# Kernel optimization log

Measured on AMD Instinct MI355X. Metric: run time of the kernel, lower is better.

Reference implementation:

```python
import jax, jax.numpy as jnp
import numpy as np

N = 50000
E = 800000
DESC = 256
IN_CH = DESC + 64  # 320
HEADS = 4
HC = 64  # hidden_channels // heads
HID = HEADS * HC  # 256


def _lin(k, fan_in, fan_out):
    kw, kb = jax.random.split(k)
    s = 1.0 / np.sqrt(fan_in)
    W = jax.random.uniform(kw, (fan_in, fan_out), minval=-s, maxval=s, dtype=jnp.float32)
    b = jax.random.uniform(kb, (fan_out,), minval=-s, maxval=s, dtype=jnp.float32)
    return W, b


def setup_inputs() -> dict:
    key = jax.random.key(0)
    ks = jax.random.split(key, 16)
    x = jax.random.normal(ks[0], (N, DESC), dtype=jnp.float32)
    kpts = jax.random.uniform(ks[1], (N, 2), dtype=jnp.float32) * jnp.array([1216.0, 352.0])
    pts_3d = jax.random.uniform(ks[2], (N, 3), dtype=jnp.float32) * 10.0
    edge_index = jax.random.randint(ks[3], (2, E), 0, N, dtype=jnp.int64)

    W1, b1 = _lin(ks[4], 3, 32)
    W2, b2 = _lin(ks[5], 32, 64)
    Wres, bres = _lin(ks[6], IN_CH, HID)
    Wl, bl = _lin(ks[7], IN_CH, HID)
    Wr, br = _lin(ks[8], IN_CH, HID)
    We, _ = _lin(ks[9], 3, HID)
    att = jax.random.normal(ks[10], (HEADS, HC), dtype=jnp.float32) * 0.1
    conv_bias = jnp.zeros((HID,), dtype=jnp.float32)
    gamma = jnp.ones((HID,), dtype=jnp.float32)
    beta = jnp.zeros((HID,), dtype=jnp.float32)
    Wp, bp = _lin(ks[11], HID, 256)
    return dict(x=x, kpts=kpts, pts_3d=pts_3d, edge_index=edge_index,
                W1=W1, b1=b1, W2=W2, b2=b2, Wres=Wres, bres=bres,
                Wl=Wl, bl=bl, Wr=Wr, br=br, We=We, att=att, conv_bias=conv_bias,
                gamma=gamma, beta=beta, Wp=Wp, bp=bp)


def reference(x, kpts, pts_3d, edge_index, W1, b1, W2, b2, Wres, bres,
              Wl, bl, Wr, br, We, att, conv_bias, gamma, beta, Wp, bp):
    n = x.shape[0]
    norm_uv = kpts / jnp.array([1216.0, 352.0], dtype=kpts.dtype)
    depth = pts_3d[:, 2:3]
    pos_input = jnp.concatenate([norm_uv, depth], axis=-1)  # [N,3]
    pos_feat = jax.nn.silu(pos_input @ W1 + b1) @ W2 + b2   # [N,64]
    node_x = jnp.concatenate([x, pos_feat], axis=-1)        # [N,320]

    src, dst = edge_index[0], edge_index[1]
    rel_uv = norm_uv[dst] - norm_uv[src]                    # [E,2]
    dist = jnp.linalg.norm(rel_uv, axis=-1, keepdims=True)  # [E,1]
    edge_attr = jnp.concatenate([rel_uv, dist], axis=-1)    # [E,3]

    identity = node_x @ Wres + bres                         # [N,256]

    # GATv2Conv (share_weights=False, concat=True, neg_slope=0.2, no self-loops)
    x_l = (node_x @ Wl + bl).reshape(n, HEADS, HC)
    x_r = (node_x @ Wr + br).reshape(n, HEADS, HC)
    e_feat = (edge_attr @ We).reshape(-1, HEADS, HC)        # [E,H,C]

    m = x_l[src] + x_r[dst] + e_feat                        # [E,H,C]
    m = jnp.where(m >= 0, m, 0.2 * m)                       # LeakyReLU(0.2)
    logits = jnp.einsum('ehc,hc->eh', m, att)               # [E,H]

    # segment softmax over incoming edges of each dst node
    lmax = jax.ops.segment_max(logits, dst, num_segments=n)  # [N,H]
    ex = jnp.exp(logits - lmax[dst])
    denom = jax.ops.segment_sum(ex, dst, num_segments=n)     # [N,H]
    alpha = ex / (denom[dst] + 1e-16)                        # [E,H]

    msg = x_l[src] * alpha[:, :, None]                       # [E,H,C]
    out = jax.ops.segment_sum(msg, dst, num_segments=n).reshape(n, HID) + conv_bias

    # LayerNorm
    mu = out.mean(-1, keepdims=True)
    var = out.var(-1, keepdims=True)
    out = (out - mu) / jnp.sqrt(var + 1e-5) * gamma + beta

    out = jax.nn.silu(out)
    out = out + identity
    out = out @ Wp + bp
    return out, alpha
```

## Files before the change

### kernel.cpp

```cpp
#include <hip/hip_runtime.h>
#include <math.h>

#define NN 50000
#define NPAD 50048
#define EE 800000
#define HIDC 256
#define INCH 320

typedef __attribute__((ext_vector_type(8))) short bf16x8;
typedef __attribute__((ext_vector_type(4))) float f32x4;
typedef __attribute__((ext_vector_type(2))) float f32x2;

static __device__ __forceinline__ float4 ld4(const float* p){ return *(const float4*)p; }

static __device__ __forceinline__ unsigned short f2b(float f){
  union { float f; unsigned u; } v; v.f = f;
  unsigned r = v.u + 0x7fffu + ((v.u >> 16) & 1u);
  return (unsigned short)(r >> 16);
}
static __device__ __forceinline__ float b2f(unsigned short u){
  union { unsigned u; float f; } v; v.u = ((unsigned)u) << 16; return v.f;
}
static __device__ __forceinline__ float rlane_f(float v, int l){
  return __uint_as_float(__builtin_amdgcn_readlane(__float_as_uint(v), l));
}
static __device__ __forceinline__ int rlane_i(int v, int l){
  return __builtin_amdgcn_readlane(v, l);
}
static __device__ __forceinline__ f32x2 unpk(unsigned u){
  f32x2 r;
  r.x = __uint_as_float(u << 16);
  r.y = __uint_as_float(u & 0xffff0000u);
  return r;
}
static __device__ __forceinline__ f32x2 fma2(f32x2 a, f32x2 b, f32x2 c){
  return __builtin_elementwise_fma(a, b, c);
}
static __device__ __forceinline__ f32x2 max2(f32x2 a, f32x2 b){
  return __builtin_elementwise_max(a, b);
}
static __device__ __forceinline__ f32x2 set2(float v){ f32x2 r; r.x = v; r.y = v; return r; }

typedef const __attribute__((address_space(1))) unsigned int* gas_u32;
typedef __attribute__((address_space(3))) unsigned int* las_u32;
static __device__ __forceinline__ void gload_lds16(const void* g, void* l){
  __builtin_amdgcn_global_load_lds((gas_u32)g, (las_u32)l, 16, 0, 0);
}

__global__ void cvt_x_kernel(const float* __restrict__ x, unsigned short* __restrict__ nodex)
{
  int t = blockIdx.x*blockDim.x + threadIdx.x;
  int row = t >> 6;
  if (row >= NN) return;
  int c4 = (t & 63) * 4;
  float4 v = ld4(x + (size_t)row*256 + c4);
  ushort4 o;
  o.x = f2b(v.x); o.y = f2b(v.y); o.z = f2b(v.z); o.w = f2b(v.w);
  *(ushort4*)(nodex + (size_t)row*320 + c4) = o;
}

__global__ void node_mlp_kernel(const float* __restrict__ kpts,
                                const float* __restrict__ pts3d,
                                const float* __restrict__ W1, const float* __restrict__ b1,
                                const float* __restrict__ W2, const float* __restrict__ b2,
                                unsigned short* __restrict__ nodex,
                                float* __restrict__ nuv)
{
  int i = blockIdx.x*blockDim.x + threadIdx.x;
  if (i >= NN) return;
  float u = kpts[2*i]   * (1.0f/1216.0f);
  float v = kpts[2*i+1] * (1.0f/352.0f);
  float d = pts3d[3*i+2];
  float2 uv; uv.x = u; uv.y = v;
  *(float2*)(nuv + 2*i) = uv;
  float h[32];
#pragma unroll
  for (int j=0;j<32;++j){
    float t = u*W1[j] + v*W1[32+j] + d*W1[64+j] + b1[j];
    h[j] = t / (1.0f + __expf(-t));
  }
  for (int o=0;o<64;o+=4){
    float s0=b2[o], s1=b2[o+1], s2=b2[o+2], s3=b2[o+3];
#pragma unroll
    for (int j=0;j<32;++j){
      float hj = h[j];
      const float* w = W2 + j*64 + o;
      s0 += hj*w[0]; s1 += hj*w[1]; s2 += hj*w[2]; s3 += hj*w[3];
    }
    ushort4 r; r.x=f2b(s0); r.y=f2b(s1); r.z=f2b(s2); r.w=f2b(s3);
    *(ushort4*)(nodex + (size_t)i*320 + 256 + o) = r;
  }
}

__global__ void cvt_w_kernel(const float* __restrict__ Wres, const float* __restrict__ Wl,
                             const float* __restrict__ Wr,   const float* __restrict__ Wp,
                             const float* __restrict__ bres, const float* __restrict__ bl,
                             const float* __restrict__ br,
                             unsigned short* __restrict__ wt, float* __restrict__ biascat)
{
  int t = blockIdx.x*blockDim.x + threadIdx.x;
  if (t < 245760) {
    int which = t / 81920;
    int rem = t % 81920;
    int n = rem / 320, k = rem % 320;
    const float* W = (which == 0) ? Wres : (which == 1) ? Wl : Wr;
    wt[(size_t)which*81920 + rem] = f2b(W[(size_t)k*256 + n]);
  } else if (t < 311296) {
    int r = t - 245760;
    int n = r / 256, k = r % 256;
    wt[245760 + r] = f2b(Wp[(size_t)k*256 + n]);
  } else {
    int r = t - 311296;
    const float* src = (r < 256) ? bres : (r < 512) ? bl : br;
    biascat[r] = src[r & 255];
  }
}

#define GK 64
__global__ __launch_bounds__(256) void mfma_gemm_kernel(
    const unsigned short* __restrict__ A,
    const unsigned short* __restrict__ BT,
    const float* __restrict__ bias,
    float* __restrict__ Cf,
    unsigned short* __restrict__ Cx1,
    unsigned short* __restrict__ Cx2,
    int M, int K)
{
  __shared__ unsigned short Als[128*GK];
  __shared__ unsigned short Bls[128*GK];
  int tid = threadIdx.x;
  int lane = tid & 63, wave = tid >> 6;
  int wm = (wave >> 1) * 64, wn = (wave & 1) * 64;
  int row0 = blockIdx.y * 128, col0 = blockIdx.x * 128;

  f32x4 acc[4][4];
#pragma unroll
  for (int i=0;i<4;++i)
#pragma unroll
    for (int j=0;j<4;++j){ acc[i][j].x=0.f; acc[i][j].y=0.f; acc[i][j].z=0.f; acc[i][j].w=0.f; }

  int fm = lane & 15;
  int q4 = lane >> 4;

  for (int k0 = 0; k0 < K; k0 += GK) {
#pragma unroll
    for (int it = 0; it < 4; ++it) {
      int cgl = it*256 + tid;
      int r = cgl >> 3;
      int kb = ((cgl ^ r) & 7) * 8;
      gload_lds16(A  + (size_t)(row0 + r)*K + k0 + kb, Als + (it*256 + wave*64)*8);
      gload_lds16(BT + (size_t)(col0 + r)*K + k0 + kb, Bls + (it*256 + wave*64)*8);
    }
    __syncthreads();

#pragma unroll
    for (int kk = 0; kk < 2; ++kk) {
      int j = kk*4 + q4;
      bf16x8 af[4], bfr[4];
#pragma unroll
      for (int mi=0; mi<4; ++mi){
        int row = wm + mi*16 + fm;
        af[mi] = *(const bf16x8*)&Als[row*GK + ((j ^ row) & 7)*8];
      }
#pragma unroll
      for (int ni=0; ni<4; ++ni){
        int row = wn + ni*16 + fm;
        bfr[ni] = *(const bf16x8*)&Bls[row*GK + ((j ^ row) & 7)*8];
      }
#pragma unroll
      for (int mi=0; mi<4; ++mi)
#pragma unroll
        for (int ni=0; ni<4; ++ni)
          acc[mi][ni] = __builtin_amdgcn_mfma_f32_16x16x32_bf16(af[mi], bfr[ni], acc[mi][ni], 0, 0, 0);
    }
    __syncthreads();
  }

  int seg = col0 >> 8;
  int colbase = col0 - seg*256;
  int cn = lane & 15, cr = (lane >> 4) * 4;
#pragma unroll
  for (int ni=0; ni<4; ++ni){
    int gcol = col0 + wn + ni*16 + cn;
    int col  = colbase + wn + ni*16 + cn;
    float bb = bias[gcol];
#pragma unroll
    for (int mi=0; mi<4; ++mi){
#pragma unroll
      for (int r=0; r<4; ++r){
        int row = row0 + wm + mi*16 + cr + r;
        if (row < M){
          float v = acc[mi][ni][r] + bb;
          if (seg == 0)      Cf [(size_t)row*256 + col] = v;
          else if (seg == 1) Cx1[(size_t)row*256 + col] = f2b(v);
          else               Cx2[(size_t)row*256 + col] = f2b(v);
        }
      }
    }
  }
}

__global__ void hist_kernel(const int* __restrict__ ei, int* __restrict__ deg){
  int e = blockIdx.x*blockDim.x + threadIdx.x;
  if (e < EE) atomicAdd(&deg[ei[EE + e]], 1);
}

__global__ __launch_bounds__(1024) void scan1_kernel(const int* __restrict__ deg,
                                                     int* __restrict__ incl, int* __restrict__ bsum){
  __shared__ int wsums[16];
  int t = threadIdx.x, lane = t & 63, w = t >> 6;
  int i = blockIdx.x*1024 + t;
  int v = (i < NN) ? deg[i] : 0;
  int sc = v;
#pragma unroll
  for (int off = 1; off < 64; off <<= 1) {
    int o = __shfl_up(sc, off, 64);
    if (lane >= off) sc += o;
  }
  if (lane == 63) wsums[w] = sc;
  __syncthreads();
  if (w == 0) {
    int ws = (lane < 16) ? wsums[lane] : 0;
#pragma unroll
    for (int off = 1; off < 16; off <<= 1) {
      int o = __shfl_up(ws, off, 64);
      if (lane >= off) ws += o;
    }
    if (lane < 16) wsums[lane] = ws;
  }
  __syncthreads();
  int woff = (w > 0) ? wsums[w-1] : 0;
  if (i < NN) incl[i] = sc + woff;
  if (t == 1023) bsum[blockIdx.x] = woff + sc;
}

__global__ void scan2_kernel(int* __restrict__ bsum, int nblk){
  int lane = threadIdx.x;
  int v = (lane < nblk) ? bsum[lane] : 0;
#pragma unroll
  for (int off = 1; off < 64; off <<= 1) {
    int o = __shfl_up(v, off, 64);
    if (lane >= off) v += o;
  }
  if (lane < nblk) bsum[lane] = v;
}

__global__ __launch_bounds__(1024) void scan3_kernel(const int* __restrict__ incl,
                                                     const int* __restrict__ deg,
                                                     const int* __restrict__ bsum,
                                                     int* __restrict__ rowptr, int* __restrict__ cursor,
                                                     int nblk){
  int i = blockIdx.x*1024 + threadIdx.x;
  if (i < NN) {
    int b = blockIdx.x;
    int prev = (b > 0) ? bsum[b-1] : 0;
    int ex = prev + incl[i] - deg[i];
    rowptr[i] = ex;
    cursor[i] = ex;
  }
  if (i == 0) rowptr[NN] = bsum[nblk-1];
}

__global__ void scatter_kernel(const int* __restrict__ ei,
                               int* __restrict__ cursor,
                               uint2* __restrict__ sedata){
  int e = blockIdx.x*blockDim.x + threadIdx.x;
  if (e >= EE) return;
  int s = ei[e];
  int d = ei[EE + e];
  int pos = atomicAdd(&cursor[d], 1);
  uint2 se; se.x = (unsigned)s; se.y = (unsigned)e;
  sedata[pos] = se;
}

#define LOAD8(Q, B0)                                               \
  if ((B0) < cnt) {                                                \
    _Pragma("unroll")                                              \
    for (int t = 0; t < 8; ++t) {                                  \
      int sj = rlane_i(s, ((B0) + t) & 63);                        \
      Q[t] = *(const uint2*)(xlp + ((size_t)sj << 8));             \
    }                                                              \
  }

#define PROC8(Q, B0)                                               \
  _Pragma("unroll")                                                \
  for (int t = 0; t < 8; ++t) {                                    \
    int j = (B0) + t;                                              \
    if (j < cnt) {                                                 \
      float ruj = rlane_f(edx, j);                                 \
      float rvj = rlane_f(edy, j);                                 \
      float dj  = rlane_f(edz, j);                                 \
      f32x2 x01 = unpk(Q[t].x), x23 = unpk(Q[t].y);                \
      f32x2 t01 = fma2(set2(ruj), we0a, xr01);                     \
      t01 = fma2(set2(rvj), we1a, t01);                            \
      t01 = fma2(set2(dj),  we2a, t01);                            \
      t01 = t01 + x01;                                             \
      f32x2 t23 = fma2(set2(ruj), we0b, xr23);                     \
      t23 = fma2(set2(rvj), we1b, t23);                            \
      t23 = fma2(set2(dj),  we2b, t23);                            \
      t23 = t23 + x23;                                             \
      t01 = max2(t01, t01*0.2f);                                   \
      t23 = max2(t23, t23*0.2f);                                   \
      f32x2 pd = t01*atta;                                         \
      pd = fma2(t23, attb, pd);                                    \
      float p = pd.x + pd.y;                                       \
      p += __shfl_xor(p, 1, 64);                                   \
      p += __shfl_xor(p, 2, 64);                                   \
      p += __shfl_xor(p, 4, 64);                                   \
      p += __shfl_xor(p, 8, 64);                                   \
      float exv = __expf(p);                                       \
      denom += exv;                                                \
      int ej = rlane_i(e, j);                                      \
      if ((lane & 15) == 0) alpha_out[(size_t)ej*4 + head] = exv;  \
      f32x2 ex2 = set2(exv);                                       \
      agg01 = fma2(ex2, x01, agg01);                               \
      agg23 = fma2(ex2, x23, agg23);                               \
    }                                                              \
  }

__global__ __launch_bounds__(128) void node_attn_kernel(
    const uint2* __restrict__ sedata, const float* __restrict__ nuv,
    const unsigned short* __restrict__ xl, const unsigned short* __restrict__ xr,
    const float* __restrict__ We, const float* __restrict__ att,
    const float* __restrict__ cbias, const float* __restrict__ gamma,
    const float* __restrict__ beta,
    const int* __restrict__ rowptr,
    const float* __restrict__ identity,
    float* __restrict__ alpha_out, float* __restrict__ denom_buf,
    unsigned short* __restrict__ hbuf)
{
  int wid  = threadIdx.x >> 6;
  int lane = threadIdx.x & 63;
  int v = blockIdx.x*2 + wid;
  if (v >= NN) return;
  int c0 = lane*4;
  int head = lane >> 4;

  f32x2 we0a, we0b, we1a, we1b, we2a, we2b, atta, attb;
  we0a.x = We[c0];       we0a.y = We[c0+1];       we0b.x = We[c0+2];       we0b.y = We[c0+3];
  we1a.x = We[256+c0];   we1a.y = We[256+c0+1];   we1b.x = We[256+c0+2];   we1b.y = We[256+c0+3];
  we2a.x = We[512+c0];   we2a.y = We[512+c0+1];   we2b.x = We[512+c0+2];   we2b.y = We[512+c0+3];
  atta.x = att[c0];      atta.y = att[c0+1];      attb.x = att[c0+2];      attb.y = att[c0+3];
  uint2 xrq = *(const uint2*)(xr + (size_t)v*256 + c0);
  f32x2 xr01 = unpk(xrq.x), xr23 = unpk(xrq.y);
  const unsigned short* xlp = xl + c0;
  float2 duv = *(const float2*)(nuv + 2*(size_t)v);

  int rs = rowptr[v], re = rowptr[v+1];
  int deg = re - rs;

  float denom = 0.f;
  f32x2 agg01 = set2(0.f), agg23 = set2(0.f);

  for (int base = 0; base < deg; base += 64) {
    int cnt = min(64, deg - base);
    int s = 0, e = 0;
    if (lane < cnt) {
      uint2 se = sedata[rs + base + lane];
      s = (int)se.x;
      e = (int)se.y;
    }
    float2 suv = *(const float2*)(nuv + 2*(size_t)s);
    float edx = duv.x - suv.x;
    float edy = duv.y - suv.y;
    float edz = sqrtf(edx*edx + edy*edy);

    uint2 qa[8], qb[8];
    LOAD8(qa, 0);
    for (int b0 = 0; b0 < cnt; b0 += 16) {
      LOAD8(qb, b0 + 8);
      PROC8(qa, b0);
      LOAD8(qa, b0 + 16);
      PROC8(qb, b0 + 8);
    }
  }

  float rdenom = 1.0f / (denom + 1e-16f);
  if ((lane & 15) == 0) denom_buf[(size_t)v*4 + head] = denom;

  float a0 = agg01.x*rdenom + cbias[c0];
  float a1 = agg01.y*rdenom + cbias[c0+1];
  float a2 = agg23.x*rdenom + cbias[c0+2];
  float a3 = agg23.y*rdenom + cbias[c0+3];

  float ps  = a0 + a1 + a2 + a3;
  float ps2 = a0*a0 + a1*a1 + a2*a2 + a3*a3;
#pragma unroll
  for (int off = 1; off < 64; off <<= 1) {
    ps  += __shfl_xor(ps,  off, 64);
    ps2 += __shfl_xor(ps2, off, 64);
  }
  float mu  = ps  * (1.0f/256.0f);
  float var = ps2 * (1.0f/256.0f) - mu*mu;
  float rstd = rsqrtf(var + 1e-5f);
  float4 g  = ld4(gamma + c0);
  float4 b  = ld4(beta  + c0);
  float4 idv = ld4(identity + (size_t)v*256 + c0);
  float y0 = (a0 - mu)*rstd*g.x + b.x;
  float y1 = (a1 - mu)*rstd*g.y + b.y;
  float y2 = (a2 - mu)*rstd*g.z + b.z;
  float y3 = (a3 - mu)*rstd*g.w + b.w;
  y0 = y0 / (1.0f + __expf(-y0)) + idv.x;
  y1 = y1 / (1.0f + __expf(-y1)) + idv.y;
  y2 = y2 / (1.0f + __expf(-y2)) + idv.z;
  y3 = y3 / (1.0f + __expf(-y3)) + idv.w;
  ushort4 hq; hq.x=f2b(y0); hq.y=f2b(y1); hq.z=f2b(y2); hq.w=f2b(y3);
  *(ushort4*)(hbuf + (size_t)v*256 + c0) = hq;
}

__global__ void alpha_fin_kernel(const int* __restrict__ ei, const float* __restrict__ denom_buf,
                                 float* __restrict__ alpha)
{
  int e = blockIdx.x*blockDim.x + threadIdx.x;
  if (e >= EE) return;
  int d = ei[EE + e];
  float4 dn = ld4(denom_buf + (size_t)d*4);
  float4 a = ld4(alpha + (size_t)e*4);
  a.x /= (dn.x + 1e-16f);
  a.y /= (dn.y + 1e-16f);
  a.z /= (dn.z + 1e-16f);
  a.w /= (dn.w + 1e-16f);
  *(float4*)(alpha + (size_t)e*4) = a;
}

extern "C" void kernel_launch(void* const* d_in, const int* in_sizes, int n_in,
                              void* d_out, int out_size, void* d_ws, size_t ws_size,
                              hipStream_t stream)
{
  const float* x      = (const float*)d_in[0];
  const float* kpts   = (const float*)d_in[1];
  const float* pts3d  = (const float*)d_in[2];
  const int*   ei     = (const int*)d_in[3];
  const float* W1     = (const float*)d_in[4];
  const float* b1     = (const float*)d_in[5];
  const float* W2     = (const float*)d_in[6];
  const float* b2     = (const float*)d_in[7];
  const float* Wres   = (const float*)d_in[8];
  const float* bres   = (const float*)d_in[9];
  const float* Wl     = (const float*)d_in[10];
  const float* bl     = (const float*)d_in[11];
  const float* Wr     = (const float*)d_in[12];
  const float* br     = (const float*)d_in[13];
  const float* We     = (const float*)d_in[14];
  const float* att    = (const float*)d_in[15];
  const float* cbias  = (const float*)d_in[16];
  const float* gamma  = (const float*)d_in[17];
  const float* beta   = (const float*)d_in[18];
  const float* Wp     = (const float*)d_in[19];
  const float* bp     = (const float*)d_in[20];

  float* out       = (float*)d_out;
  float* alpha_out = out + (size_t)NN*HIDC;

  float* wsf = (float*)d_ws;
  float*          identity = wsf;
  unsigned short* xl       = (unsigned short*)(wsf + 12800000);
  unsigned short* xr       = (unsigned short*)(wsf + 19206144);
  unsigned short* nodex    = (unsigned short*)(wsf + 25612288);
  unsigned short* hbuf     = (unsigned short*)(wsf + 25612288);
  unsigned short* wt       = (unsigned short*)(wsf + 33619968);
  float*          biascat  = wsf + 33775616;
  float*          denomb   = wsf + 33776384;
  uint2*          sedata   = (uint2*)(wsf + 33976384);
  float*          nuv      = wsf + 35576384;
  int*            incl     = (int*)(wsf + 37176384);
  int*            deg      = (int*)(wsf + 37976384);
  int*            rowptr   = (int*)(wsf + 38026384);
  int*            cursor   = (int*)(wsf + 38076385);
  int*            bsum     = (int*)(wsf + 38126385);

  unsigned short* wtcat = wt;
  unsigned short* wtp   = wt + 245760;

  cvt_x_kernel<<<12500, 256, 0, stream>>>(x, nodex);
  node_mlp_kernel<<<(NN+255)/256, 256, 0, stream>>>(kpts, pts3d, W1, b1, W2, b2, nodex, nuv);
  cvt_w_kernel<<<1219, 256, 0, stream>>>(Wres, Wl, Wr, Wp, bres, bl, br, wt, biascat);

  dim3 g3(6, NPAD/128);
  mfma_gemm_kernel<<<g3, 256, 0, stream>>>(nodex, wtcat, biascat, identity, xl, xr, NN, INCH);

  hipMemsetAsync(deg, 0, NN*sizeof(int), stream);
  hist_kernel<<<(EE+255)/256, 256, 0, stream>>>(ei, deg);
  int nblk = (NN + 1023) / 1024;
  scan1_kernel<<<nblk, 1024, 0, stream>>>(deg, incl, bsum);
  scan2_kernel<<<1, 64, 0, stream>>>(bsum, nblk);
  scan3_kernel<<<nblk, 1024, 0, stream>>>(incl, deg, bsum, rowptr, cursor, nblk);
  scatter_kernel<<<(EE+255)/256, 256, 0, stream>>>(ei, cursor, sedata);

  node_attn_kernel<<<(NN+1)/2, 128, 0, stream>>>(sedata, nuv, xl, xr, We, att,
                                                 cbias, gamma, beta,
                                                 rowptr, identity,
                                                 alpha_out, denomb, hbuf);
  alpha_fin_kernel<<<(EE+255)/256, 256, 0, stream>>>(ei, denomb, alpha_out);

  dim3 g1(2, NPAD/128);
  mfma_gemm_kernel<<<g1, 256, 0, stream>>>(hbuf, wtp, bp, out, nullptr, nullptr, NN, HIDC);
}
```

Baseline: 537.0 us.

## Merge prep kernels, single-block scan, fold alpha normalization into attention kernel

Result: slower. 583.1 us (+8.6%).

```diff
diff --git a/kernel.cpp b/kernel.cpp
--- a/kernel.cpp
+++ b/kernel.cpp
@@ -47,72 +47,73 @@
   __builtin_amdgcn_global_load_lds((gas_u32)g, (las_u32)l, 16, 0, 0);
 }
 
-__global__ void cvt_x_kernel(const float* __restrict__ x, unsigned short* __restrict__ nodex)
+#define PREP_CVTX  12500
+#define PREP_MLP   196
+#define PREP_CVTW  1219
+__global__ __launch_bounds__(256) void prep_kernel(
+    const float* __restrict__ x, unsigned short* __restrict__ nodex,
+    const float* __restrict__ kpts, const float* __restrict__ pts3d,
+    const float* __restrict__ W1, const float* __restrict__ b1,
+    const float* __restrict__ W2, const float* __restrict__ b2,
+    float* __restrict__ nuv, int* __restrict__ deg,
+    const float* __restrict__ Wres, const float* __restrict__ Wl,
+    const float* __restrict__ Wr,  const float* __restrict__ Wp,
+    const float* __restrict__ bres, const float* __restrict__ bl,
+    const float* __restrict__ br,
+    unsigned short* __restrict__ wt, float* __restrict__ biascat)
 {
-  int t = blockIdx.x*blockDim.x + threadIdx.x;
-  int row = t >> 6;
-  if (row >= NN) return;
-  int c4 = (t & 63) * 4;
-  float4 v = ld4(x + (size_t)row*256 + c4);
-  ushort4 o;
-  o.x = f2b(v.x); o.y = f2b(v.y); o.z = f2b(v.z); o.w = f2b(v.w);
-  *(ushort4*)(nodex + (size_t)row*320 + c4) = o;
-}
-
-__global__ void node_mlp_kernel(const float* __restrict__ kpts,
-                                const float* __restrict__ pts3d,
-                                const float* __restrict__ W1, const float* __restrict__ b1,
-                                const float* __restrict__ W2, const float* __restrict__ b2,
-                                unsigned short* __restrict__ nodex,
-                                float* __restrict__ nuv)
-{
-  int i = blockIdx.x*blockDim.x + threadIdx.x;
-  if (i >= NN) return;
-  float u = kpts[2*i]   * (1.0f/1216.0f);
-  float v = kpts[2*i+1] * (1.0f/352.0f);
-  float d = pts3d[3*i+2];
-  float2 uv; uv.x = u; uv.y = v;
-  *(float2*)(nuv + 2*i) = uv;
-  float h[32];
-#pragma unroll
-  for (int j=0;j<32;++j){
-    float t = u*W1[j] + v*W1[32+j] + d*W1[64+j] + b1[j];
-    h[j] = t / (1.0f + __expf(-t));
-  }
-  for (int o=0;o<64;o+=4){
-    float s0=b2[o], s1=b2[o+1], s2=b2[o+2], s3=b2[o+3];
+  int b = blockIdx.x;
+  if (b < PREP_CVTX) {
+    int t = b*256 + threadIdx.x;
+    int row = t >> 6;
+    int c4 = (t & 63) * 4;
+    float4 v = ld4(x + (size_t)row*256 + c4);
+    ushort4 o;
+    o.x = f2b(v.x); o.y = f2b(v.y); o.z = f2b(v.z); o.w = f2b(v.w);
+    *(ushort4*)(nodex + (size_t)row*320 + c4) = o;
+  } else if (b < PREP_CVTX + PREP_MLP) {
+    int i = (b - PREP_CVTX)*256 + threadIdx.x;
+    if (i >= NN) return;
+    deg[i] = 0;
+    float u = kpts[2*i]   * (1.0f/1216.0f);
+    float v = kpts[2*i+1] * (1.0f/352.0f);
+    float d = pts3d[3*i+2];
+    float2 uv; uv.x = u; uv.y = v;
+    *(float2*)(nuv + 2*i) = uv;
+    float h[32];
 #pragma unroll
     for (int j=0;j<32;++j){
-      float hj = h[j];
-      const float* w = W2 + j*64 + o;
-      s0 += hj*w[0]; s1 += hj*w[1]; s2 += hj*w[2]; s3 += hj*w[3];
-    }
-    ushort4 r; r.x=f2b(s0); r.y=f2b(s1); r.z=f2b(s2); r.w=f2b(s3);
-    *(ushort4*)(nodex + (size_t)i*320 + 256 + o) = r;
-  }
-}
-
-__global__ void cvt_w_kernel(const float* __restrict__ Wres, const float* __restrict__ Wl,
-                             const float* __restrict__ Wr,   const float* __restrict__ Wp,
-                             const float* __restrict__ bres, const float* __restrict__ bl,
-                             const float* __restrict__ br,
-                             unsigned short* __restrict__ wt, float* __restrict__ biascat)
-{
-  int t = blockIdx.x*blockDim.x + threadIdx.x;
-  if (t < 245760) {
-    int which = t / 81920;
-    int rem = t % 81920;
-    int n = rem / 320, k = rem % 320;
-    const float* W = (which == 0) ? Wres : (which == 1) ? Wl : Wr;
-    wt[(size_t)which*81920 + rem] = f2b(W[(size_t)k*256 + n]);
-  } else if (t < 311296) {
-    int r = t - 245760;
-    int n = r / 256, k = r % 256;
-    wt[245760 + r] = f2b(Wp[(size_t)k*256 + n]);
+      float t = u*W1[j] + v*W1[32+j] + d*W1[64+j] + b1[j];
+      h[j] = t / (1.0f + __expf(-t));
+    }
+    for (int o=0;o<64;o+=4){
+      float s0=b2[o], s1=b2[o+1], s2=b2[o+2], s3=b2[o+3];
+#pragma unroll
+      for (int j=0;j<32;++j){
+        float hj = h[j];
+        const float* w = W2 + j*64 + o;
+        s0 += hj*w[0]; s1 += hj*w[1]; s2 += hj*w[2]; s3 += hj*w[3];
+      }
+      ushort4 r; r.x=f2b(s0); r.y=f2b(s1); r.z=f2b(s2); r.w=f2b(s3);
+      *(ushort4*)(nodex + (size_t)i*320 + 256 + o) = r;
+    }
   } else {
-    int r = t - 311296;
-    const float* src = (r < 256) ? bres : (r < 512) ? bl : br;
-    biascat[r] = src[r & 255];
+    int t = (b - PREP_CVTX - PREP_MLP)*256 + threadIdx.x;
+    if (t < 245760) {
+      int which = t / 81920;
+      int rem = t % 81920;
+      int n = rem / 320, k = rem % 320;
+      const float* W = (which == 0) ? Wres : (which == 1) ? Wl : Wr;
+      wt[(size_t)which*81920 + rem] = f2b(W[(size_t)k*256 + n]);
+    } else if (t < 311296) {
+      int r = t - 245760;
+      int n = r / 256, k = r % 256;
+      wt[245760 + r] = f2b(Wp[(size_t)k*256 + n]);
+    } else if (t < 312064) {
+      int r = t - 311296;
+      const float* src = (r < 256) ? bres : (r < 512) ? bl : br;
+      biascat[r] = src[r & 255];
+    }
   }
 }
 
@@ -205,60 +206,45 @@
   if (e < EE) atomicAdd(&deg[ei[EE + e]], 1);
 }
 
-__global__ __launch_bounds__(1024) void scan1_kernel(const int* __restrict__ deg,
-                                                     int* __restrict__ incl, int* __restrict__ bsum){
+__global__ __launch_bounds__(1024) void scan_all_kernel(const int* __restrict__ deg,
+                                                        int* __restrict__ rowptr,
+                                                        int* __restrict__ cursor)
+{
   __shared__ int wsums[16];
   int t = threadIdx.x, lane = t & 63, w = t >> 6;
-  int i = blockIdx.x*1024 + t;
-  int v = (i < NN) ? deg[i] : 0;
-  int sc = v;
-#pragma unroll
-  for (int off = 1; off < 64; off <<= 1) {
-    int o = __shfl_up(sc, off, 64);
-    if (lane >= off) sc += o;
-  }
-  if (lane == 63) wsums[w] = sc;
-  __syncthreads();
-  if (w == 0) {
-    int ws = (lane < 16) ? wsums[lane] : 0;
-#pragma unroll
-    for (int off = 1; off < 16; off <<= 1) {
-      int o = __shfl_up(ws, off, 64);
-      if (lane >= off) ws += o;
-    }
-    if (lane < 16) wsums[lane] = ws;
-  }
-  __syncthreads();
-  int woff = (w > 0) ? wsums[w-1] : 0;
-  if (i < NN) incl[i] = sc + woff;
-  if (t == 1023) bsum[blockIdx.x] = woff + sc;
-}
-
-__global__ void scan2_kernel(int* __restrict__ bsum, int nblk){
-  int lane = threadIdx.x;
-  int v = (lane < nblk) ? bsum[lane] : 0;
-#pragma unroll
-  for (int off = 1; off < 64; off <<= 1) {
-    int o = __shfl_up(v, off, 64);
-    if (lane >= off) v += o;
-  }
-  if (lane < nblk) bsum[lane] = v;
-}
-
-__global__ __launch_bounds__(1024) void scan3_kernel(const int* __restrict__ incl,
-                                                     const int* __restrict__ deg,
-                                                     const int* __restrict__ bsum,
-                                                     int* __restrict__ rowptr, int* __restrict__ cursor,
-                                                     int nblk){
-  int i = blockIdx.x*1024 + threadIdx.x;
-  if (i < NN) {
-    int b = blockIdx.x;
-    int prev = (b > 0) ? bsum[b-1] : 0;
-    int ex = prev + incl[i] - deg[i];
-    rowptr[i] = ex;
-    cursor[i] = ex;
-  }
-  if (i == 0) rowptr[NN] = bsum[nblk-1];
+  int carry = 0;
+  for (int c = 0; c < (NN + 1023)/1024; ++c) {
+    int i = c*1024 + t;
+    int v = (i < NN) ? deg[i] : 0;
+    int sc = v;
+#pragma unroll
+    for (int off = 1; off < 64; off <<= 1) {
+      int o = __shfl_up(sc, off, 64);
+      if (lane >= off) sc += o;
+    }
+    if (lane == 63) wsums[w] = sc;
+    __syncthreads();
+    if (w == 0) {
+      int ws = (lane < 16) ? wsums[lane] : 0;
+#pragma unroll
+      for (int off = 1; off < 16; off <<= 1) {
+        int o = __shfl_up(ws, off, 64);
+        if (lane >= off) ws += o;
+      }
+      if (lane < 16) wsums[lane] = ws;
+    }
+    __syncthreads();
+    int woff = (w > 0) ? wsums[w-1] : 0;
+    int btot = wsums[15];
+    if (i < NN) {
+      int ex = carry + woff + sc - v;
+      rowptr[i] = ex;
+      cursor[i] = ex;
+    }
+    carry += btot;
+    __syncthreads();
+  }
+  if (t == 0) rowptr[NN] = carry;
 }
 
 __global__ void scatter_kernel(const int* __restrict__ ei,
@@ -326,7 +312,7 @@
     const float* __restrict__ beta,
     const int* __restrict__ rowptr,
     const float* __restrict__ identity,
-    float* __restrict__ alpha_out, float* __restrict__ denom_buf,
+    float* __restrict__ alpha_out,
     unsigned short* __restrict__ hbuf)
 {
   int wid  = threadIdx.x >> 6;
@@ -375,8 +361,19 @@
     }
   }
 
+  float dd0 = rlane_f(denom, 0)  + 1e-16f;
+  float dd1 = rlane_f(denom, 16) + 1e-16f;
+  float dd2 = rlane_f(denom, 32) + 1e-16f;
+  float dd3 = rlane_f(denom, 48) + 1e-16f;
+  asm volatile("s_waitcnt vmcnt(0)" ::: "memory");
+  for (int j = lane; j < deg; j += 64) {
+    unsigned e = sedata[rs + j].y;
+    float4 a = *(float4*)(alpha_out + (size_t)e*4);
+    a.x /= dd0; a.y /= dd1; a.z /= dd2; a.w /= dd3;
+    *(float4*)(alpha_out + (size_t)e*4) = a;
+  }
+
   float rdenom = 1.0f / (denom + 1e-16f);
-  if ((lane & 15) == 0) denom_buf[(size_t)v*4 + head] = denom;
 
   float a0 = agg01.x*rdenom + cbias[c0];
   float a1 = agg01.y*rdenom + cbias[c0+1];
@@ -406,21 +403,6 @@
   y3 = y3 / (1.0f + __expf(-y3)) + idv.w;
   ushort4 hq; hq.x=f2b(y0); hq.y=f2b(y1); hq.z=f2b(y2); hq.w=f2b(y3);
   *(ushort4*)(hbuf + (size_t)v*256 + c0) = hq;
-}
-
-__global__ void alpha_fin_kernel(const int* __restrict__ ei, const float* __restrict__ denom_buf,
-                                 float* __restrict__ alpha)
-{
-  int e = blockIdx.x*blockDim.x + threadIdx.x;
-  if (e >= EE) return;
-  int d = ei[EE + e];
-  float4 dn = ld4(denom_buf + (size_t)d*4);
-  float4 a = ld4(alpha + (size_t)e*4);
-  a.x /= (dn.x + 1e-16f);
-  a.y /= (dn.y + 1e-16f);
-  a.z /= (dn.z + 1e-16f);
-  a.w /= (dn.w + 1e-16f);
-  *(float4*)(alpha + (size_t)e*4) = a;
 }
 
 extern "C" void kernel_launch(void* const* d_in, const int* in_sizes, int n_in,
@@ -460,38 +442,32 @@
   unsigned short* hbuf     = (unsigned short*)(wsf + 25612288);
   unsigned short* wt       = (unsigned short*)(wsf + 33619968);
   float*          biascat  = wsf + 33775616;
-  float*          denomb   = wsf + 33776384;
   uint2*          sedata   = (uint2*)(wsf + 33976384);
   float*          nuv      = wsf + 35576384;
-  int*            incl     = (int*)(wsf + 37176384);
   int*            deg      = (int*)(wsf + 37976384);
   int*            rowptr   = (int*)(wsf + 38026384);
   int*            cursor   = (int*)(wsf + 38076385);
-  int*            bsum     = (int*)(wsf + 38126385);
 
   unsigned short* wtcat = wt;
   unsigned short* wtp   = wt + 245760;
 
-  cvt_x_kernel<<<12500, 256, 0, stream>>>(x, nodex);
-  node_mlp_kernel<<<(NN+255)/256, 256, 0, stream>>>(kpts, pts3d, W1, b1, W2, b2, nodex, nuv);
-  cvt_w_kernel<<<1219, 256, 0, stream>>>(Wres, Wl, Wr, Wp, bres, bl, br, wt, biascat);
+  prep_kernel<<<PREP_CVTX + PREP_MLP + PREP_CVTW, 256, 0, stream>>>(
+      x, nodex, kpts, pts3d, W1, b1, W2, b2, nuv, deg,
+      Wres, Wl, Wr, Wp, bres, bl, br, wt, biascat);
 
   dim3 g3(6, NPAD/128);
   mfma_gemm_kernel<<<g3, 256, 0, stream>>>(nodex, wtcat, biascat, identity, xl, xr, NN, INCH);
 
-  hipMemsetAsync(deg, 0, NN*sizeof(int), stream);
   hist_kernel<<<(EE+255)/256, 256, 0, stream>>>(ei, deg);
-  int nblk = (NN + 1023) / 1024;
-  scan1_kernel<<<nblk, 1024, 0, stream>>>(deg, incl, bsum);
-  scan2_kernel<<<1, 64, 0, stream>>>(bsum, nblk);
-  scan3_kernel<<<nblk, 1024, 0, stream>>>(incl, deg, bsum, rowptr, cursor, nblk);
+
+  scan_all_kernel<<<1, 1024, 0, stream>>>(deg, rowptr, cursor);
+
   scatter_kernel<<<(EE+255)/256, 256, 0, stream>>>(ei, cursor, sedata);
 
   node_attn_kernel<<<(NN+1)/2, 128, 0, stream>>>(sedata, nuv, xl, xr, We, att,
                                                  cbias, gamma, beta,
                                                  rowptr, identity,
-                                                 alpha_out, denomb, hbuf);
-  alpha_fin_kernel<<<(EE+255)/256, 256, 0, stream>>>(ei, denomb, alpha_out);
+                                                 alpha_out, hbuf);
 
   dim3 g1(2, NPAD/128);
   mfma_gemm_kernel<<<g1, 256, 0, stream>>>(hbuf, wtp, bp, out, nullptr, nullptr, NN, HIDC);
```
